# Kernel tuning notes

Measured on AMD Instinct MI355X. Metric: run time of the kernel, lower is better.

## Reference

```python
import jax, jax.numpy as jnp
import numpy as np

K = 20
EPS = 1e-5


def _bn(h, g, b, axes):
    m = jnp.mean(h, axes, keepdims=True)
    v = jnp.var(h, axes, keepdims=True)
    return (h - m) * jax.lax.rsqrt(v + EPS) * g + b


def _edge_feat(h):
    # h: [B,N,D] -> edge features [B,N,K,2D] = concat(central, neighbor-central)
    sq = jnp.sum(h * h, -1)
    # negative squared pairwise distance (larger = closer)
    adj = 2.0 * jnp.einsum('bnd,bmd->bnm', h, h) - sq[:, :, None] - sq[:, None, :]
    idx = jax.lax.top_k(adj, K)[1]  # [B,N,K] nearest (incl. self)
    nbr = jax.vmap(lambda hb, ib: hb[ib])(h, idx)  # [B,N,K,D]
    ctr = jnp.broadcast_to(h[:, :, None, :], nbr.shape)
    return jnp.concatenate([ctr, nbr - ctr], -1)


def _edge_layer(h, W, b, g, be):
    # 1x1 conv over edge features, relu THEN batchnorm (matches torch: bn(relu(conv))), max over K
    ef = _edge_feat(h)
    z = jax.nn.relu(jnp.einsum('bnkc,oc->bnko', ef, W) + b)
    z = _bn(z, g, be, (0, 1, 2))
    return jnp.max(z, axis=2)  # [B,N,O]


def _c1d(h, W, b):
    return jnp.einsum('bcl,oc->bol', h, W) + b[None, :, None]


def _bnc(h, g, b):
    m = jnp.mean(h, (0, 2), keepdims=True)
    v = jnp.var(h, (0, 2), keepdims=True)
    return (h - m) * jax.lax.rsqrt(v + EPS) * g[None, :, None] + b[None, :, None]


def _forward(x, rand_grid, W1, b1, g1, be1, W2, b2, g2, be2, W3, b3, g3, be3,
             W4, b4, g4, be4, W5, b5, g5, be5, lW, lb, lg, lbe,
             dW1, db1, dg1, dbe1, dW2, db2, dg2, dbe2, dW3, db3, dg3, dbe3, dW4, db4):
    pts = jnp.transpose(x, (0, 2, 1))  # [B,N,3]
    x1 = _edge_layer(pts, W1, b1, g1, be1)   # [B,N,64]
    x2 = _edge_layer(x1, W2, b2, g2, be2)    # [B,N,64]
    x3 = _edge_layer(x2, W3, b3, g3, be3)    # [B,N,64]
    x4 = _edge_layer(x3, W4, b4, g4, be4)    # [B,N,128]
    cat = jnp.concatenate([x1, x2, x3, x4], -1)  # [B,N,320]
    z = jax.nn.relu(jnp.einsum('bnc,oc->bno', cat, W5) + b5)
    z = _bn(z, g5, be5, (0, 1))
    glob = jnp.max(z, axis=1)  # [B,1024]
    lat = glob @ lW.T + lb
    lat = jax.nn.relu(_bn(lat, lg, lbe, (0,)))  # [B,1024]
    B, C = lat.shape
    P = rand_grid.shape[2]
    y = jnp.concatenate([rand_grid, jnp.broadcast_to(lat[:, :, None], (B, C, P))], axis=1)  # [B,1026,P]
    h = jax.nn.relu(_bnc(_c1d(y, dW1, db1), dg1, dbe1))
    h = jax.nn.relu(_bnc(_c1d(h, dW2, db2), dg2, dbe2))
    h = jax.nn.relu(_bnc(_c1d(h, dW3, db3), dg3, dbe3))
    return jnp.tanh(_c1d(h, dW4, db4))  # [B,3,P]


def setup_inputs() -> dict:
    key = jax.random.key(0)
    ks = iter(jax.random.split(key, 64))
    B, N, BOT = 8, 2048, 1024
    D = BOT + 2  # 1026
    f32 = jnp.float32

    def w(o, c):
        return jax.random.normal(next(ks), (o, c), dtype=f32) * 0.05

    def bnp(c):
        return jnp.ones((c,), f32), jnp.zeros((c,), f32)

    inp = {
        'x': jax.random.normal(next(ks), (B, 3, N), dtype=f32),
        'rand_grid': jax.random.uniform(next(ks), (B, 2, N), dtype=f32),
    }
    enc = [(64, 6), (64, 128), (64, 128), (128, 128), (1024, 320)]
    for i, (o, c) in enumerate(enc, 1):
        inp[f'W{i}'] = w(o, c)
        inp[f'b{i}'] = jnp.zeros((o,), f32)
        inp[f'g{i}'], inp[f'be{i}'] = bnp(o)
    inp['lW'] = w(BOT, 1024)
    inp['lb'] = jnp.zeros((BOT,), f32)
    inp['lg'], inp['lbe'] = bnp(BOT)
    dec = [(D, D), (D // 2, D), (D // 4, D // 2), (3, D // 4)]
    for i, (o, c) in enumerate(dec, 1):
        inp[f'dW{i}'] = w(o, c)
        inp[f'db{i}'] = jnp.zeros((o,), f32)
        if i < 4:
            inp[f'dg{i}'], inp[f'dbe{i}'] = bnp(o)
    return inp


def reference(x, rand_grid, W1, b1, g1, be1, W2, b2, g2, be2, W3, b3, g3, be3,
              W4, b4, g4, be4, W5, b5, g5, be5, lW, lb, lg, lbe,
              dW1, db1, dg1, dbe1, dW2, db2, dg2, dbe2, dW3, db3, dg3, dbe3, dW4, db4):
    return _forward(x, rand_grid, W1, b1, g1, be1, W2, b2, g2, be2, W3, b3, g3, be3,
                    W4, b4, g4, be4, W5, b5, g5, be5, lW, lb, lg, lbe,
                    dW1, db1, dg1, dbe1, dW2, db2, dg2, dbe2, dW3, db3, dg3, dbe3, dW4, db4)
```

## Files before the change

kernel.cpp:

```cpp
#include <hip/hip_runtime.h>
#include <math.h>

constexpr int NB = 8;
constexpr int NN = 2048;
constexpr int NK = 20;
constexpr int NP = 2048;


__global__ void transpose_x_kernel(const float* __restrict__ x, float* __restrict__ pts) {
  int gid = blockIdx.x * 256 + threadIdx.x;
  if (gid >= NB * NN * 3) return;
  int c = gid % 3;
  int n = (gid / 3) % NN;
  int b = gid / (3 * NN);
  pts[gid] = x[(b * 3 + c) * NN + n];
}

__global__ void transpose_mat_ld(const float* __restrict__ src, float* __restrict__ dst, int R,
                                 int C, int ldd) {
  __shared__ float tile[32][33];
  int c0 = blockIdx.x * 32, r0 = blockIdx.y * 32;
  int tx = threadIdx.x & 31, ty = threadIdx.x >> 5;
  for (int i = ty; i < 32; i += 8) {
    int r = r0 + i, c = c0 + tx;
    tile[i][tx] = (r < R && c < C) ? src[(size_t)r * C + c] : 0.f;
  }
  __syncthreads();
  for (int i = ty; i < 32; i += 8) {
    int c = c0 + i, r = r0 + tx;
    if (r < R && c < C) dst[(size_t)c * ldd + r] = tile[tx][i];
  }
}

template <int D>
__global__ void knn_dist_kernel(const float* __restrict__ h, int ld, int coff, int b0,
                                float* __restrict__ dmat) {
  __shared__ float sc[64][4];
  __shared__ float sr[64][4];
  int t = threadIdx.x;
  int c0 = blockIdx.x * 64;
  int r0 = blockIdx.y * 512;
  int bz = blockIdx.z;
  const float* rows = h + ((size_t)(b0 + bz) * NN) * ld + coff;
  if (t < 192) {
    int r = t / 3, c = t - r * 3;
    sc[r][c] = rows[(size_t)(c0 + r) * ld + c];
  }
  int tx = t & 15, ty = t >> 4;
  for (int rt = 0; rt < 8; rt++) {
    int rr0 = r0 + rt * 64;
    __syncthreads();
    if (t < 192) {
      int r = t / 3, c = t - r * 3;
      sr[r][c] = rows[(size_t)(rr0 + r) * ld + c];
    }
    __syncthreads();
    float acc[4][4] = {};
    float ca[4][3], rb[4][3];
#pragma unroll
    for (int i = 0; i < 4; i++)
#pragma unroll
      for (int d = 0; d < 3; d++) ca[i][d] = sc[ty + 16 * i][d];
#pragma unroll
    for (int j = 0; j < 4; j++)
#pragma unroll
      for (int d = 0; d < 3; d++) rb[j][d] = sr[tx + 16 * j][d];
#pragma unroll
    for (int i = 0; i < 4; i++)
#pragma unroll
      for (int j = 0; j < 4; j++)
#pragma unroll
        for (int d = 0; d < 3; d++) {
          float dd = ca[i][d] - rb[j][d];
          acc[i][j] = fmaf(dd, dd, acc[i][j]);
        }
#pragma unroll
    for (int i = 0; i < 4; i++)
#pragma unroll
      for (int j = 0; j < 4; j++)
        dmat[((size_t)bz * NN + c0 + ty + 16 * i) * NN + rr0 + tx + 16 * j] = -acc[i][j];
  }
}

__global__ __launch_bounds__(256, 2) void knn_dist128_kernel(const float* __restrict__ h, int ld,
                                                             int coff, int b0,
                                                             float* __restrict__ dmat) {
  __shared__ float sc[16][132];
  __shared__ float sr[16][128];
  int t = threadIdx.x;
  int c0 = blockIdx.x * 128, r0 = blockIdx.y * 128;
  int bz = blockIdx.z;
  const float* rows = h + ((size_t)(b0 + bz) * NN) * ld + coff;
  int arow = t >> 1, ac = (t & 1) * 8;
  int tx = t & 15, ty = t >> 4;
  float acc[8][8] = {};
  float rA[8], rB[8];

  auto gload = [&](int d0) {
    const float* pc = &rows[(size_t)(c0 + arow) * ld + d0 + ac];
    float4 a0 = *(const float4*)pc;
    float4 a1 = *(const float4*)(pc + 4);
    rA[0] = a0.x; rA[1] = a0.y; rA[2] = a0.z; rA[3] = a0.w;
    rA[4] = a1.x; rA[5] = a1.y; rA[6] = a1.z; rA[7] = a1.w;
    const float* pr = &rows[(size_t)(r0 + arow) * ld + d0 + ac];
    float4 b0 = *(const float4*)pr;
    float4 b1 = *(const float4*)(pr + 4);
    rB[0] = b0.x; rB[1] = b0.y; rB[2] = b0.z; rB[3] = b0.w;
    rB[4] = b1.x; rB[5] = b1.y; rB[6] = b1.z; rB[7] = b1.w;
  };
  auto ldswrite = [&]() {
#pragma unroll
    for (int j = 0; j < 8; j++) {
      sc[ac + j][arow] = rA[j];
      sr[ac + j][arow] = rB[j];
    }
  };

  gload(0);
  for (int ks = 0; ks < 4; ks++) {
    __syncthreads();
    ldswrite();
    __syncthreads();
    if (ks + 1 < 4) gload((ks + 1) * 16);
#pragma unroll
    for (int d = 0; d < 16; d++) {
      float4 a0 = *(const float4*)&sc[d][ty * 4];
      float4 a1 = *(const float4*)&sc[d][64 + ty * 4];
      float4 b0 = *(const float4*)&sr[d][tx * 4];
      float4 b1 = *(const float4*)&sr[d][64 + tx * 4];
      float av[8] = {a0.x, a0.y, a0.z, a0.w, a1.x, a1.y, a1.z, a1.w};
      float bv[8] = {b0.x, b0.y, b0.z, b0.w, b1.x, b1.y, b1.z, b1.w};
#pragma unroll
      for (int i = 0; i < 8; i++)
#pragma unroll
        for (int j = 0; j < 8; j++) {
          float dd = av[i] - bv[j];
          acc[i][j] = fmaf(dd, dd, acc[i][j]);
        }
    }
  }
#pragma unroll
  for (int i = 0; i < 8; i++) {
    int c = c0 + (i < 4 ? ty * 4 + i : 64 + ty * 4 + (i - 4));
    float* dst = &dmat[((size_t)bz * NN + c) * NN + r0];
    float4 q0, q1;
    q0.x = -acc[i][0]; q0.y = -acc[i][1]; q0.z = -acc[i][2]; q0.w = -acc[i][3];
    q1.x = -acc[i][4]; q1.y = -acc[i][5]; q1.z = -acc[i][6]; q1.w = -acc[i][7];
    *(float4*)&dst[tx * 4] = q0;
    *(float4*)&dst[64 + tx * 4] = q1;
  }
}

__global__ void knn_topk_kernel(const float* __restrict__ dmat, int b0, int* __restrict__ idx) {
  int t = threadIdx.x;
  int l = t & 63;
  int w = t >> 6;
  int gr = blockIdx.x * 4 + w;
  int bz = gr >> 11;
  int n = gr & 2047;
  const float* row = dmat + ((size_t)bz * NN + n) * NN;
  float v[32];
#pragma unroll
  for (int j = 0; j < 32; j++) v[j] = row[j * 64 + l];
  int mykm = 0;
  for (int k = 0; k < NK; k++) {
    float bv = v[0];
    int bj = 0;
#pragma unroll
    for (int j = 1; j < 32; j++) {
      if (v[j] > bv) { bv = v[j]; bj = j; }
    }
    int gm = bj * 64 + l;
#pragma unroll
    for (int off = 32; off; off >>= 1) {
      float ov = __shfl_xor(bv, off, 64);
      int om = __shfl_xor(gm, off, 64);
      if (ov > bv || (ov == bv && om < gm)) { bv = ov; gm = om; }
    }
    if (l == k) mykm = gm;
    int jb = gm >> 6, lb = gm & 63;
#pragma unroll
    for (int j = 0; j < 32; j++)
      if (j == jb && l == lb) v[j] = -3e38f;
  }
  if (l < NK) idx[((size_t)((b0 + bz) * NN + n)) * NK + l] = mykm;
}

__global__ void weff_kernel(const float* __restrict__ W, int O, int D, float* __restrict__ Weff) {
  int i = blockIdx.x * 256 + threadIdx.x;
  if (i >= 2 * O * D) return;
  int o = i / D, d = i - o * D;
  float v;
  if (o < O) v = W[(size_t)o * 2 * D + d] - W[(size_t)o * 2 * D + D + d];
  else v = W[(size_t)(o - O) * 2 * D + D + d];
  Weff[i] = v;
}

template <int M2, int D>
__global__ __launch_bounds__(256, 4) void pgemm_kernel(const float* __restrict__ h, int ld,
                                                       int coff, const float* __restrict__ Weff,
                                                       const float* __restrict__ bias,
                                                       float* __restrict__ P) {
  constexpr int O = M2 / 2;
  constexpr int GRP = 256 / M2;
  constexpr int NR = 8 / GRP;
  __shared__ float sh[8][D == 3 ? 4 : 68];
  int t = threadIdx.x;
  int n0 = blockIdx.x * 8;
  const float* base = h + coff;
  if constexpr (D == 64) {
    if (t < 128) {
      int r = t >> 4, q = (t & 15) * 4;
      *(float4*)&sh[r][q] = *(const float4*)&base[(size_t)(n0 + r) * ld + q];
    }
  } else {
    if (t < 24) {
      int r = t / 3, c = t - r * 3;
      sh[r][c] = base[(size_t)(n0 + r) * ld + c];
    }
  }
  __syncthreads();
  int o = t % M2;
  int gi = t / M2;
  float acc[NR];
  float bz = (o < O) ? bias[o] : 0.f;
#pragma unroll
  for (int j = 0; j < NR; j++) acc[j] = bz;
  const float* wr = Weff + (size_t)o * D;
  if constexpr (D == 64) {
#pragma unroll
    for (int d4 = 0; d4 < 16; d4++) {
      float4 w4 = *(const float4*)&wr[d4 * 4];
#pragma unroll
      for (int j = 0; j < NR; j++) {
        float4 e4 = *(const float4*)&sh[gi * NR + j][d4 * 4];
        acc[j] = fmaf(w4.x, e4.x, acc[j]);
        acc[j] = fmaf(w4.y, e4.y, acc[j]);
        acc[j] = fmaf(w4.z, e4.z, acc[j]);
        acc[j] = fmaf(w4.w, e4.w, acc[j]);
      }
    }
  } else {
    float w0 = wr[0], w1 = wr[1], w2 = wr[2];
#pragma unroll
    for (int j = 0; j < NR; j++) {
      int r = gi * NR + j;
      acc[j] = fmaf(w0, sh[r][0], fmaf(w1, sh[r][1], fmaf(w2, sh[r][2], acc[j])));
    }
  }
#pragma unroll
  for (int j = 0; j < NR; j++)
    P[(size_t)(n0 + gi * NR + j) * M2 + o] = acc[j];
}

template <int O>
__global__ __launch_bounds__(256, 8) void combine_kernel(const float* __restrict__ P,
                                                         const int* __restrict__ idx,
                                                         float* __restrict__ zmax,
                                                         float* __restrict__ zmin,
                                                         float* __restrict__ psum,
                                                         float* __restrict__ psq) {
  constexpr int CPB = 256 / O;
  constexpr int M2 = 2 * O;
  __shared__ int sidx[CPB * NK];
  int t = threadIdx.x;
  int bn0 = blockIdx.x * CPB;
  if (t < CPB * NK) sidx[t] = idx[(size_t)bn0 * NK + t];
  __syncthreads();
  int g = t / O, o = t % O;
  int bn = bn0 + g;
  int b = bn >> 11;
  float p1 = P[(size_t)bn * M2 + o];
  const float* P2 = P + (size_t)b * NN * M2 + O + o;
  float s = 0.f, sq = 0.f, mx = -3e38f, mn = 3e38f;
#pragma unroll
  for (int k = 0; k < NK; k++) {
    int nb = sidx[g * NK + k];
    float z = fmaxf(p1 + P2[(size_t)nb * M2], 0.f);
    s += z;
    sq = fmaf(z, z, sq);
    mx = fmaxf(mx, z);
    mn = fminf(mn, z);
  }
  zmax[(size_t)bn * O + o] = mx;
  zmin[(size_t)bn * O + o] = mn;
  psum[(size_t)o * (NB * NN) + bn] = s;
  psq[(size_t)o * (NB * NN) + bn] = sq;
}

__global__ void edge_reduce_kernel(const float* __restrict__ psum, const float* __restrict__ psq,
                                   const float* __restrict__ g, const float* __restrict__ be,
                                   float* __restrict__ scale, float* __restrict__ shift,
                                   double inv_n) {
  int o = blockIdx.x, t = threadIdx.x;
  double s = 0.0, q = 0.0;
  const float* ps = psum + (size_t)o * (NB * NN);
  const float* pq = psq + (size_t)o * (NB * NN);
  for (int i = t; i < NB * NN; i += 256) { s += (double)ps[i]; q += (double)pq[i]; }
  __shared__ double rs[256], rq[256];
  rs[t] = s; rq[t] = q;
  __syncthreads();
  for (int st = 128; st; st >>= 1) {
    if (t < st) { rs[t] += rs[t + st]; rq[t] += rq[t + st]; }
    __syncthreads();
  }
  if (t == 0) {
    double mean = rs[0] * inv_n;
    double var = rq[0] * inv_n - mean * mean;
    double r = 1.0 / sqrt(var + 1e-5);
    double sc = (double)g[o] * r;
    scale[o] = (float)sc;
    shift[o] = (float)((double)be[o] - mean * sc);
  }
}

__global__ void edge_affine_kernel(const float* __restrict__ zmax, const float* __restrict__ zmin,
                                   const float* __restrict__ scale, const float* __restrict__ shift,
                                   float* __restrict__ cat, int O, int coff_out) {
  int gid = blockIdx.x * 256 + threadIdx.x;
  int o = gid % O;
  int bn = gid / O;
  float sc = scale[o];
  float v = (sc >= 0.f) ? zmax[gid] : zmin[gid];
  cat[(size_t)bn * 320 + coff_out + o] = fmaf(sc, v, shift[o]);
}

__global__ __launch_bounds__(256, 2) void gemm5_64_kernel(const float* __restrict__ cat,
                                                          const float* __restrict__ W5t,
                                                          const float* __restrict__ b5,
                                                          float* __restrict__ z5) {
  __shared__ float sA[16][64];
  __shared__ float sB[16][128];
  int t = threadIdx.x;
  int r0 = blockIdx.x * 64, m0 = blockIdx.y * 128;
  int arow = t & 63, acq = (t >> 6) * 4;
  int blr = t >> 4, blc = (t & 15) * 8;
  int tx = t & 15, ty = t >> 4;
  float acc[4][8] = {};
  float rA[4], rB[8];

  auto gload = [&](int c0) {
    float4 a = *(const float4*)&cat[(size_t)(r0 + arow) * 320 + c0 + acq];
    rA[0] = a.x; rA[1] = a.y; rA[2] = a.z; rA[3] = a.w;
    const float* pb = &W5t[(size_t)(c0 + blr) * 1024 + m0 + blc];
    float4 b0 = *(const float4*)pb;
    float4 b1 = *(const float4*)(pb + 4);
    rB[0] = b0.x; rB[1] = b0.y; rB[2] = b0.z; rB[3] = b0.w;
    rB[4] = b1.x; rB[5] = b1.y; rB[6] = b1.z; rB[7] = b1.w;
  };
  auto ldswrite = [&]() {
#pragma unroll
    for (int j = 0; j < 4; j++) sA[acq + j][arow] = rA[j];
    float4 w0, w1;
    w0.x = rB[0]; w0.y = rB[1]; w0.z = rB[2]; w0.w = rB[3];
    w1.x = rB[4]; w1.y = rB[5]; w1.z = rB[6]; w1.w = rB[7];
    *(float4*)&sB[blr][blc] = w0;
    *(float4*)&sB[blr][blc + 4] = w1;
  };

  gload(0);
  for (int kt = 0; kt < 20; kt++) {
    __syncthreads();
    ldswrite();
    __syncthreads();
    if (kt + 1 < 20) gload((kt + 1) * 16);
#pragma unroll
    for (int c = 0; c < 16; c++) {
      float4 a0 = *(const float4*)&sA[c][ty * 4];
      float4 b0 = *(const float4*)&sB[c][tx * 4];
      float4 b1 = *(const float4*)&sB[c][64 + tx * 4];
      float av[4] = {a0.x, a0.y, a0.z, a0.w};
      float bv[8] = {b0.x, b0.y, b0.z, b0.w, b1.x, b1.y, b1.z, b1.w};
#pragma unroll
      for (int i = 0; i < 4; i++)
#pragma unroll
        for (int j = 0; j < 8; j++) acc[i][j] = fmaf(av[i], bv[j], acc[i][j]);
    }
  }
  float bj[8];
#pragma unroll
  for (int j = 0; j < 8; j++)
    bj[j] = b5[m0 + (j < 4 ? tx * 4 + j : 64 + tx * 4 + (j - 4))];
#pragma unroll
  for (int i = 0; i < 4; i++) {
    int r = r0 + ty * 4 + i;
    float* dst = &z5[(size_t)r * 1024 + m0];
    float4 q0, q1;
    q0.x = fmaxf(acc[i][0] + bj[0], 0.f);
    q0.y = fmaxf(acc[i][1] + bj[1], 0.f);
    q0.z = fmaxf(acc[i][2] + bj[2], 0.f);
    q0.w = fmaxf(acc[i][3] + bj[3], 0.f);
    q1.x = fmaxf(acc[i][4] + bj[4], 0.f);
    q1.y = fmaxf(acc[i][5] + bj[5], 0.f);
    q1.z = fmaxf(acc[i][6] + bj[6], 0.f);
    q1.w = fmaxf(acc[i][7] + bj[7], 0.f);
    *(float4*)&dst[tx * 4] = q0;
    *(float4*)&dst[64 + tx * 4] = q1;
  }
}

__global__ void stats5_kernel(const float* __restrict__ z5, double* __restrict__ psum5,
                              double* __restrict__ psq5, float* __restrict__ pmax5,
                              float* __restrict__ pmin5) {
  int j = blockIdx.x, t = threadIdx.x;
  int row0 = j * 64;
  double s0 = 0, s1 = 0, s2 = 0, s3 = 0, q0 = 0, q1 = 0, q2 = 0, q3 = 0;
  float4 mx = {-3e38f, -3e38f, -3e38f, -3e38f}, mn = {3e38f, 3e38f, 3e38f, 3e38f};
  for (int r = 0; r < 64; r++) {
    float4 v = *(const float4*)&z5[(size_t)(row0 + r) * 1024 + t * 4];
    s0 += v.x; s1 += v.y; s2 += v.z; s3 += v.w;
    q0 += (double)v.x * v.x; q1 += (double)v.y * v.y;
    q2 += (double)v.z * v.z; q3 += (double)v.w * v.w;
    mx.x = fmaxf(mx.x, v.x); mx.y = fmaxf(mx.y, v.y); mx.z = fmaxf(mx.z, v.z); mx.w = fmaxf(mx.w, v.w);
    mn.x = fminf(mn.x, v.x); mn.y = fminf(mn.y, v.y); mn.z = fminf(mn.z, v.z); mn.w = fminf(mn.w, v.w);
  }
  size_t base = (size_t)j * 1024 + t * 4;
  psum5[base + 0] = s0; psum5[base + 1] = s1; psum5[base + 2] = s2; psum5[base + 3] = s3;
  psq5[base + 0] = q0; psq5[base + 1] = q1; psq5[base + 2] = q2; psq5[base + 3] = q3;
  *(float4*)&pmax5[base] = mx;
  *(float4*)&pmin5[base] = mn;
}

__global__ void reduce5_glob_kernel(const double* __restrict__ psum5, const double* __restrict__ psq5,
                                    const float* __restrict__ pmax5, const float* __restrict__ pmin5,
                                    const float* __restrict__ g5, const float* __restrict__ be5,
                                    float* __restrict__ glob) {
  int o = blockIdx.x * 256 + threadIdx.x;
  double s = 0.0, q = 0.0;
  for (int j = 0; j < 256; j++) {
    s += psum5[(size_t)j * 1024 + o];
    q += psq5[(size_t)j * 1024 + o];
  }
  double mean = s * (1.0 / 16384.0);
  double var = q * (1.0 / 16384.0) - mean * mean;
  double r = 1.0 / sqrt(var + 1e-5);
  double scd = (double)g5[o] * r;
  float sc = (float)scd;
  float sh = (float)((double)be5[o] - mean * scd);
  for (int b = 0; b < 8; b++) {
    float m;
    if (sc >= 0.f) {
      m = -3e38f;
      for (int jj = 0; jj < 32; jj++) m = fmaxf(m, pmax5[(size_t)(b * 32 + jj) * 1024 + o]);
    } else {
      m = 3e38f;
      for (int jj = 0; jj < 32; jj++) m = fminf(m, pmin5[(size_t)(b * 32 + jj) * 1024 + o]);
    }
    glob[b * 1024 + o] = fmaf(sc, m, sh);
  }
}

__global__ void fc_kernel(const float* __restrict__ in, const float* __restrict__ Wt, int ld,
                          int coff, const float* __restrict__ bias, float* __restrict__ out,
                          int Ci, int Co) {
  __shared__ float sin_[1024];
  __shared__ float red[8][32];
  int b = blockIdx.x, t = threadIdx.x;
  for (int e = t; e < Ci; e += 256) sin_[e] = in[(size_t)b * Ci + e];
  __syncthreads();
  int o = blockIdx.y * 32 + (t & 31);
  int cg = t >> 5;
  int cn = Ci / 8;
  float p = 0.f;
  if (o < Co) {
    for (int c = cg * cn; c < (cg + 1) * cn; c++)
      p = fmaf(Wt[(size_t)(c + coff) * ld + o], sin_[c], p);
  }
  red[cg][t & 31] = p;
  __syncthreads();
  if (cg == 0 && o < Co) {
    float s = red[0][t] + red[1][t] + red[2][t] + red[3][t] + red[4][t] + red[5][t] + red[6][t] +
              red[7][t];
    out[(size_t)b * Co + o] = s + bias[o];
  }
}

__global__ void lat_bn_kernel(const float* __restrict__ latp, const float* __restrict__ lg,
                              const float* __restrict__ lbe, float* __restrict__ lat) {
  int o = blockIdx.x * 256 + threadIdx.x;
  float v[8];
  double s = 0.0, q = 0.0;
  for (int b = 0; b < 8; b++) {
    v[b] = latp[b * 1024 + o];
    s += (double)v[b];
    q += (double)v[b] * (double)v[b];
  }
  double mean = s * 0.125;
  double var = q * 0.125 - mean * mean;
  double r = 1.0 / sqrt(var + 1e-5);
  double gd = (double)lg[o], bd = (double)lbe[o];
  for (int b = 0; b < 8; b++) {
    float z = (float)(((double)v[b] - mean) * r * gd + bd);
    lat[b * 1024 + o] = fmaxf(z, 0.f);
  }
}

__global__ void dec1_z_kernel(const float* __restrict__ rg, const float* __restrict__ dW1t,
                              const float* __restrict__ u, float* __restrict__ z1) {
  int bo = blockIdx.x;
  int b = bo / 1026;
  int o = bo - b * 1026;
  int t = threadIdx.x;
  float w0 = dW1t[o], w1 = dW1t[1026 + o], ub = u[bo];
  const float4* r0 = (const float4*)(rg + (size_t)b * 2 * NP);
  const float4* r1 = (const float4*)(rg + (size_t)b * 2 * NP + NP);
  float4* zr = (float4*)(z1 + (size_t)bo * NP);
  for (int i = t; i < NP / 4; i += 256) {
    float4 a = r0[i], c = r1[i], rr;
    rr.x = fmaf(w0, a.x, fmaf(w1, c.x, ub));
    rr.y = fmaf(w0, a.y, fmaf(w1, c.y, ub));
    rr.z = fmaf(w0, a.z, fmaf(w1, c.z, ub));
    rr.w = fmaf(w0, a.w, fmaf(w1, c.w, ub));
    zr[i] = rr;
  }
}

__global__ void dstats_kernel(const float* __restrict__ z, int C, const float* __restrict__ g,
                              const float* __restrict__ be, float* __restrict__ scale,
                              float* __restrict__ shift) {
  int o = blockIdx.x, t = threadIdx.x;
  double s = 0.0, q = 0.0;
  for (int b = 0; b < 8; b++) {
    const float4* row = (const float4*)(z + ((size_t)b * C + o) * NP);
    for (int i = t; i < NP / 4; i += 256) {
      float4 v = row[i];
      s += (double)v.x + (double)v.y + (double)v.z + (double)v.w;
      q += (double)v.x * v.x + (double)v.y * v.y + (double)v.z * v.z + (double)v.w * v.w;
    }
  }
  __shared__ double rs[256], rq[256];
  rs[t] = s; rq[t] = q;
  __syncthreads();
  for (int st = 128; st; st >>= 1) {
    if (t < st) { rs[t] += rs[t + st]; rq[t] += rq[t + st]; }
    __syncthreads();
  }
  if (t == 0) {
    double inv = 1.0 / (8.0 * NP);
    double mean = rs[0] * inv;
    double var = rq[0] * inv - mean * mean;
    double r = 1.0 / sqrt(var + 1e-5);
    double sc = (double)g[o] * r;
    scale[o] = (float)sc;
    shift[o] = (float)((double)be[o] - mean * sc);
  }
}

__global__ __launch_bounds__(256, 2) void dec_gemm64_kernel(
    const float* __restrict__ zin, const float* __restrict__ Wt, int ldA,
    const float* __restrict__ bias, const float* __restrict__ scale,
    const float* __restrict__ shift, float* __restrict__ zout, int Ci, int Co) {
  __shared__ float sA[16][64];
  __shared__ float sB[16][128];
  int t = threadIdx.x;
  int m0 = blockIdx.x * 64, p0 = blockIdx.y * 128, b = blockIdx.z;
  int lr = t >> 4, lcA = (t & 15) * 4, lcB = (t & 15) * 8;
  int tx = t & 15, ty = t >> 4;
  int numK = (Ci + 15) >> 4;
  float acc[4][8] = {};
  float rA[4], rB[8];

  auto gload = [&](int kt) {
    int c = kt * 16 + lr;
#pragma unroll
    for (int j = 0; j < 4; j++) rA[j] = 0.f;
#pragma unroll
    for (int j = 0; j < 8; j++) rB[j] = 0.f;
    if (c < Ci) {
      int mb = m0 + lcA;
      if (mb + 4 <= Co) {
        float4 a0 = *(const float4*)&Wt[(size_t)c * ldA + mb];
        rA[0] = a0.x; rA[1] = a0.y; rA[2] = a0.z; rA[3] = a0.w;
      } else {
#pragma unroll
        for (int j = 0; j < 4; j++)
          if (mb + j < Co) rA[j] = Wt[(size_t)c * ldA + mb + j];
      }
      float sc = scale[c], sh = shift[c];
      const float* src = &zin[((size_t)b * Ci + c) * NP + p0 + lcB];
      float4 z0 = *(const float4*)src;
      float4 z1 = *(const float4*)(src + 4);
      rB[0] = fmaxf(fmaf(sc, z0.x, sh), 0.f);
      rB[1] = fmaxf(fmaf(sc, z0.y, sh), 0.f);
      rB[2] = fmaxf(fmaf(sc, z0.z, sh), 0.f);
      rB[3] = fmaxf(fmaf(sc, z0.w, sh), 0.f);
      rB[4] = fmaxf(fmaf(sc, z1.x, sh), 0.f);
      rB[5] = fmaxf(fmaf(sc, z1.y, sh), 0.f);
      rB[6] = fmaxf(fmaf(sc, z1.z, sh), 0.f);
      rB[7] = fmaxf(fmaf(sc, z1.w, sh), 0.f);
    }
  };
  auto ldswrite = [&]() {
    float4 v0;
    v0.x = rA[0]; v0.y = rA[1]; v0.z = rA[2]; v0.w = rA[3];
    *(float4*)&sA[lr][lcA] = v0;
    float4 w0, w1;
    w0.x = rB[0]; w0.y = rB[1]; w0.z = rB[2]; w0.w = rB[3];
    w1.x = rB[4]; w1.y = rB[5]; w1.z = rB[6]; w1.w = rB[7];
    *(float4*)&sB[lr][lcB] = w0;
    *(float4*)&sB[lr][lcB + 4] = w1;
  };

  gload(0);
  for (int kt = 0; kt < numK; kt++) {
    __syncthreads();
    ldswrite();
    __syncthreads();
    if (kt + 1 < numK) gload(kt + 1);
#pragma unroll
    for (int c = 0; c < 16; c++) {
      float4 a0 = *(const float4*)&sA[c][ty * 4];
      float4 b0 = *(const float4*)&sB[c][tx * 4];
      float4 b1 = *(const float4*)&sB[c][64 + tx * 4];
      float av[4] = {a0.x, a0.y, a0.z, a0.w};
      float bv[8] = {b0.x, b0.y, b0.z, b0.w, b1.x, b1.y, b1.z, b1.w};
#pragma unroll
      for (int i = 0; i < 4; i++)
#pragma unroll
        for (int j = 0; j < 8; j++) acc[i][j] = fmaf(av[i], bv[j], acc[i][j]);
    }
  }
#pragma unroll
  for (int i = 0; i < 4; i++) {
    int m = m0 + ty * 4 + i;
    if (m < Co) {
      float bv = bias[m];
      float* dst = &zout[((size_t)b * Co + m) * NP + p0];
      float4 q0, q1;
      q0.x = acc[i][0] + bv; q0.y = acc[i][1] + bv;
      q0.z = acc[i][2] + bv; q0.w = acc[i][3] + bv;
      q1.x = acc[i][4] + bv; q1.y = acc[i][5] + bv;
      q1.z = acc[i][6] + bv; q1.w = acc[i][7] + bv;
      *(float4*)&dst[tx * 4] = q0;
      *(float4*)&dst[64 + tx * 4] = q1;
    }
  }
}

__global__ void dec_final_kernel(const float* __restrict__ z3, const float* __restrict__ dW4,
                                 const float* __restrict__ db4, const float* __restrict__ scale,
                                 const float* __restrict__ shift, float* __restrict__ out) {
  __shared__ float w4[3 * 256];
  __shared__ float sc[256], sh[256];
  __shared__ float red[4][64][3];
  int b = blockIdx.x, pc = blockIdx.y, t = threadIdx.x;
  for (int e = t; e < 768; e += 256) w4[e] = dW4[e];
  sc[t] = scale[t];
  sh[t] = shift[t];
  __syncthreads();
  int tp = t & 63, tc = t >> 6;
  int p = pc * 64 + tp;
  float a0 = 0.f, a1 = 0.f, a2 = 0.f;
  for (int c = tc * 64; c < tc * 64 + 64; c++) {
    float hv = fmaxf(fmaf(sc[c], z3[((size_t)(b * 256 + c)) * NP + p], sh[c]), 0.f);
    a0 = fmaf(w4[c], hv, a0);
    a1 = fmaf(w4[256 + c], hv, a1);
    a2 = fmaf(w4[512 + c], hv, a2);
  }
  red[tc][tp][0] = a0;
  red[tc][tp][1] = a1;
  red[tc][tp][2] = a2;
  __syncthreads();
  if (tc == 0) {
    a0 = red[0][tp][0] + red[1][tp][0] + red[2][tp][0] + red[3][tp][0];
    a1 = red[0][tp][1] + red[1][tp][1] + red[2][tp][1] + red[3][tp][1];
    a2 = red[0][tp][2] + red[1][tp][2] + red[2][tp][2] + red[3][tp][2];
    out[((size_t)b * 3 + 0) * NP + p] = tanhf(a0 + db4[0]);
    out[((size_t)b * 3 + 1) * NP + p] = tanhf(a1 + db4[1]);
    out[((size_t)b * 3 + 2) * NP + p] = tanhf(a2 + db4[2]);
  }
}


extern "C" void kernel_launch(void* const* d_in, const int* in_sizes, int n_in, void* d_out,
                              int out_size, void* d_ws, size_t ws_size, hipStream_t stream) {
  const float* x = (const float*)d_in[0];
  const float* rg = (const float*)d_in[1];
  const float* W1 = (const float*)d_in[2];
  const float* b1 = (const float*)d_in[3];
  const float* g1 = (const float*)d_in[4];
  const float* be1 = (const float*)d_in[5];
  const float* W2 = (const float*)d_in[6];
  const float* b2 = (const float*)d_in[7];
  const float* g2 = (const float*)d_in[8];
  const float* be2 = (const float*)d_in[9];
  const float* W3 = (const float*)d_in[10];
  const float* b3 = (const float*)d_in[11];
  const float* g3 = (const float*)d_in[12];
  const float* be3 = (const float*)d_in[13];
  const float* W4 = (const float*)d_in[14];
  const float* b4 = (const float*)d_in[15];
  const float* g4 = (const float*)d_in[16];
  const float* be4 = (const float*)d_in[17];
  const float* W5 = (const float*)d_in[18];
  const float* b5 = (const float*)d_in[19];
  const float* g5 = (const float*)d_in[20];
  const float* be5 = (const float*)d_in[21];
  const float* lW = (const float*)d_in[22];
  const float* lb = (const float*)d_in[23];
  const float* lg = (const float*)d_in[24];
  const float* lbe = (const float*)d_in[25];
  const float* dW1 = (const float*)d_in[26];
  const float* db1 = (const float*)d_in[27];
  const float* dg1 = (const float*)d_in[28];
  const float* dbe1 = (const float*)d_in[29];
  const float* dW2 = (const float*)d_in[30];
  const float* db2 = (const float*)d_in[31];
  const float* dg2 = (const float*)d_in[32];
  const float* dbe2 = (const float*)d_in[33];
  const float* dW3 = (const float*)d_in[34];
  const float* db3 = (const float*)d_in[35];
  const float* dg3 = (const float*)d_in[36];
  const float* dbe3 = (const float*)d_in[37];
  const float* dW4 = (const float*)d_in[38];
  const float* db4 = (const float*)d_in[39];
  float* out = (float*)d_out;

  float* ws = (float*)d_ws;
  size_t off = 0;
  auto alloc = [&](size_t n) {
    size_t r = off;
    off += (n + 255) & ~(size_t)255;
    return r;
  };
  size_t f_pts = alloc((size_t)NB * NN * 3);
  size_t f_uA = alloc(13959168);
  size_t f_cat = f_uA;
  size_t f_idx = f_cat + 5242880;
  size_t f_zmax = f_idx + 327680;
  size_t f_zmin = f_zmax + 2097152;
  size_t f_psum = f_zmin + 2097152;
  size_t f_psq = f_psum + 2097152;
  size_t f_z2 = f_uA;
  size_t f_uB = alloc(16809984);
  size_t f_z5 = f_uB, f_z1 = f_uB;
  float* dmat = ws + f_uB;
  float* P = ws + f_uB;
  size_t f_uC = alloc(4194304);
  double* ps5_d = (double*)(ws + f_uC);
  double* pq5_d = ps5_d + 262144;
  size_t f_pM5 = f_uC + 2097152;
  size_t f_pm5 = f_pM5 + 262144;
  size_t f_z3 = f_uC;
  size_t f_weff = alloc(256 * 64);
  size_t f_W5t = alloc(320 * 1024);
  size_t f_lWt = alloc(1024 * 1024);
  size_t f_dW1t = alloc((size_t)1026 * 1026);
  size_t f_dW2t = alloc((size_t)1026 * 516);
  size_t f_dW3t = alloc(513 * 256);
  size_t f_scale = alloc(2048);
  size_t f_shift = alloc(2048);
  size_t f_glob = alloc(8 * 1024);
  size_t f_latp = alloc(8 * 1024);
  size_t f_lat = alloc(8 * 1024);
  size_t f_u = alloc(8 * 1026);
  (void)ws_size;
  (void)in_sizes;
  (void)n_in;
  (void)out_size;

  float* cat = ws + f_cat;
  int* idxp = (int*)(ws + f_idx);
  float* zmax = ws + f_zmax;
  float* zmin = ws + f_zmin;
  float* psumf = ws + f_psum;
  float* psqf = ws + f_psq;
  float* weff = ws + f_weff;
  float* scale = ws + f_scale;
  float* shift = ws + f_shift;
  const double invn_e = 1.0 / (double)(NB * NN * NK);

  transpose_x_kernel<<<192, 256, 0, stream>>>(x, ws + f_pts);
  transpose_mat_ld<<<dim3(10, 32), 256, 0, stream>>>(W5, ws + f_W5t, 1024, 320, 1024);
  transpose_mat_ld<<<dim3(32, 32), 256, 0, stream>>>(lW, ws + f_lWt, 1024, 1024, 1024);
  transpose_mat_ld<<<dim3(33, 33), 256, 0, stream>>>(dW1, ws + f_dW1t, 1026, 1026, 1026);
  transpose_mat_ld<<<dim3(33, 17), 256, 0, stream>>>(dW2, ws + f_dW2t, 513, 1026, 516);
  transpose_mat_ld<<<dim3(17, 8), 256, 0, stream>>>(dW3, ws + f_dW3t, 256, 513, 256);

  auto run_knn = [&](const float* h, int ld, int coff, bool d64) {
    for (int bb0 = 0; bb0 < NB; bb0 += 4) {
      if (d64)
        knn_dist128_kernel<<<dim3(16, 16, 4), 256, 0, stream>>>(h, ld, coff, bb0, dmat);
      else
        knn_dist_kernel<3><<<dim3(32, 4, 4), 256, 0, stream>>>(h, ld, coff, bb0, dmat);
      knn_topk_kernel<<<2048, 256, 0, stream>>>(dmat, bb0, idxp);
    }
  };

  run_knn(ws + f_pts, 3, 0, false);
  weff_kernel<<<2, 256, 0, stream>>>(W1, 64, 3, weff);
  pgemm_kernel<128, 3><<<2048, 256, 0, stream>>>(ws + f_pts, 3, 0, weff, b1, P);
  combine_kernel<64><<<4096, 256, 0, stream>>>(P, idxp, zmax, zmin, psumf, psqf);
  edge_reduce_kernel<<<64, 256, 0, stream>>>(psumf, psqf, g1, be1, scale, shift, invn_e);
  edge_affine_kernel<<<NB * NN * 64 / 256, 256, 0, stream>>>(zmax, zmin, scale, shift, cat, 64, 0);
  run_knn(cat, 320, 0, true);
  weff_kernel<<<32, 256, 0, stream>>>(W2, 64, 64, weff);
  pgemm_kernel<128, 64><<<2048, 256, 0, stream>>>(cat, 320, 0, weff, b2, P);
  combine_kernel<64><<<4096, 256, 0, stream>>>(P, idxp, zmax, zmin, psumf, psqf);
  edge_reduce_kernel<<<64, 256, 0, stream>>>(psumf, psqf, g2, be2, scale, shift, invn_e);
  edge_affine_kernel<<<NB * NN * 64 / 256, 256, 0, stream>>>(zmax, zmin, scale, shift, cat, 64, 64);
  run_knn(cat, 320, 64, true);
  weff_kernel<<<32, 256, 0, stream>>>(W3, 64, 64, weff);
  pgemm_kernel<128, 64><<<2048, 256, 0, stream>>>(cat, 320, 64, weff, b3, P);
  combine_kernel<64><<<4096, 256, 0, stream>>>(P, idxp, zmax, zmin, psumf, psqf);
  edge_reduce_kernel<<<64, 256, 0, stream>>>(psumf, psqf, g3, be3, scale, shift, invn_e);
  edge_affine_kernel<<<NB * NN * 64 / 256, 256, 0, stream>>>(zmax, zmin, scale, shift, cat, 64, 128);
  run_knn(cat, 320, 128, true);
  weff_kernel<<<64, 256, 0, stream>>>(W4, 128, 64, weff);
  pgemm_kernel<256, 64><<<2048, 256, 0, stream>>>(cat, 320, 128, weff, b4, P);
  combine_kernel<128><<<8192, 256, 0, stream>>>(P, idxp, zmax, zmin, psumf, psqf);
  edge_reduce_kernel<<<128, 256, 0, stream>>>(psumf, psqf, g4, be4, scale, shift, invn_e);
  edge_affine_kernel<<<NB * NN * 128 / 256, 256, 0, stream>>>(zmax, zmin, scale, shift, cat, 128, 192);

  gemm5_64_kernel<<<dim3(256, 8), 256, 0, stream>>>(cat, ws + f_W5t, b5, ws + f_z5);
  stats5_kernel<<<256, 256, 0, stream>>>(ws + f_z5, ps5_d, pq5_d, ws + f_pM5, ws + f_pm5);
  reduce5_glob_kernel<<<4, 256, 0, stream>>>(ps5_d, pq5_d, ws + f_pM5, ws + f_pm5, g5, be5,
                                             ws + f_glob);
  fc_kernel<<<dim3(8, 32), 256, 0, stream>>>(ws + f_glob, ws + f_lWt, 1024, 0, lb, ws + f_latp,
                                             1024, 1024);
  lat_bn_kernel<<<4, 256, 0, stream>>>(ws + f_latp, lg, lbe, ws + f_lat);
  fc_kernel<<<dim3(8, 33), 256, 0, stream>>>(ws + f_lat, ws + f_dW1t, 1026, 2, db1, ws + f_u, 1024,
                                             1026);
  dec1_z_kernel<<<8 * 1026, 256, 0, stream>>>(rg, ws + f_dW1t, ws + f_u, ws + f_z1);
  dstats_kernel<<<1026, 256, 0, stream>>>(ws + f_z1, 1026, dg1, dbe1, scale, shift);
  dec_gemm64_kernel<<<dim3(9, 16, 8), 256, 0, stream>>>(ws + f_z1, ws + f_dW2t, 516, db2, scale,
                                                        shift, ws + f_z2, 1026, 513);
  dstats_kernel<<<513, 256, 0, stream>>>(ws + f_z2, 513, dg2, dbe2, scale, shift);
  dec_gemm64_kernel<<<dim3(4, 16, 8), 256, 0, stream>>>(ws + f_z2, ws + f_dW3t, 256, db3, scale,
                                                        shift, ws + f_z3, 513, 256);
  dstats_kernel<<<256, 256, 0, stream>>>(ws + f_z3, 256, dg3, dbe3, scale, shift);
  dec_final_kernel<<<dim3(8, 32), 256, 0, stream>>>(ws + f_z3, dW4, db4, scale, shift, out);
}
```

Before: 1.858 ms.

## Fuse 3-D kNN distance and top-k; swizzle decoder GEMM block order

The first-layer kNN on 3-D points now runs as a single kernel. It loads a whole batch's points into shared memory, each wave computes its point's 2048 distances in registers, and it selects the top 20 with wave-shuffle argmax. This removes the dense distance-matrix write and read and two launches per batch half. The decoder GEMMs also switch to a 1-D grid with a remapped block order so that groups of 8 consecutive blocks share the same M tile, for better L2 reuse of the weights. Trade-off: only 4 waves per block, each reloading the full point set from global memory, and 20 serial selection passes over 32 registers per lane.

```diff
diff --git a/kernel.cpp b/kernel.cpp
--- a/kernel.cpp
+++ b/kernel.cpp
@@ -32,54 +32,56 @@
   }
 }
 
-template <int D>
-__global__ void knn_dist_kernel(const float* __restrict__ h, int ld, int coff, int b0,
-                                float* __restrict__ dmat) {
-  __shared__ float sc[64][4];
-  __shared__ float sr[64][4];
+__global__ void knn3_fused_kernel(const float* __restrict__ pts, int* __restrict__ idx) {
+  __shared__ float sm[3][NN];
   int t = threadIdx.x;
-  int c0 = blockIdx.x * 64;
-  int r0 = blockIdx.y * 512;
-  int bz = blockIdx.z;
-  const float* rows = h + ((size_t)(b0 + bz) * NN) * ld + coff;
-  if (t < 192) {
-    int r = t / 3, c = t - r * 3;
-    sc[r][c] = rows[(size_t)(c0 + r) * ld + c];
-  }
-  int tx = t & 15, ty = t >> 4;
-  for (int rt = 0; rt < 8; rt++) {
-    int rr0 = r0 + rt * 64;
-    __syncthreads();
-    if (t < 192) {
-      int r = t / 3, c = t - r * 3;
-      sr[r][c] = rows[(size_t)(rr0 + r) * ld + c];
-    }
-    __syncthreads();
-    float acc[4][4] = {};
-    float ca[4][3], rb[4][3];
-#pragma unroll
-    for (int i = 0; i < 4; i++)
-#pragma unroll
-      for (int d = 0; d < 3; d++) ca[i][d] = sc[ty + 16 * i][d];
-#pragma unroll
-    for (int j = 0; j < 4; j++)
-#pragma unroll
-      for (int d = 0; d < 3; d++) rb[j][d] = sr[tx + 16 * j][d];
-#pragma unroll
-    for (int i = 0; i < 4; i++)
-#pragma unroll
-      for (int j = 0; j < 4; j++)
-#pragma unroll
-        for (int d = 0; d < 3; d++) {
-          float dd = ca[i][d] - rb[j][d];
-          acc[i][j] = fmaf(dd, dd, acc[i][j]);
-        }
-#pragma unroll
-    for (int i = 0; i < 4; i++)
-#pragma unroll
-      for (int j = 0; j < 4; j++)
-        dmat[((size_t)bz * NN + c0 + ty + 16 * i) * NN + rr0 + tx + 16 * j] = -acc[i][j];
-  }
+  int l = t & 63, w = t >> 6;
+  int gb = blockIdx.x;
+  int b = gb >> 9;
+  int n0 = (gb & 511) * 4;
+  const float* base = pts + (size_t)b * NN * 3;
+  for (int e = t; e < NN * 3; e += 256) {
+    int col = e / 3, d = e - col * 3;
+    sm[d][col] = base[e];
+  }
+  __syncthreads();
+  int n = n0 + w;
+  float c0 = sm[0][n], c1 = sm[1][n], c2 = sm[2][n];
+  float v[32];
+#pragma unroll
+  for (int j = 0; j < 32; j++) {
+    int col = j * 64 + l;
+    float d0 = c0 - sm[0][col];
+    float d1 = c1 - sm[1][col];
+    float d2 = c2 - sm[2][col];
+    float acc = 0.f;
+    acc = fmaf(d0, d0, acc);
+    acc = fmaf(d1, d1, acc);
+    acc = fmaf(d2, d2, acc);
+    v[j] = -acc;
+  }
+  int mykm = 0;
+  for (int k = 0; k < NK; k++) {
+    float bv = v[0];
+    int bj = 0;
+#pragma unroll
+    for (int j = 1; j < 32; j++) {
+      if (v[j] > bv) { bv = v[j]; bj = j; }
+    }
+    int gm = bj * 64 + l;
+#pragma unroll
+    for (int off = 32; off; off >>= 1) {
+      float ov = __shfl_xor(bv, off, 64);
+      int om = __shfl_xor(gm, off, 64);
+      if (ov > bv || (ov == bv && om < gm)) { bv = ov; gm = om; }
+    }
+    if (l == k) mykm = gm;
+    int jb = gm >> 6, lb = gm & 63;
+#pragma unroll
+    for (int j = 0; j < 32; j++)
+      if (j == jb && l == lb) v[j] = -3e38f;
+  }
+  if (l < NK) idx[((size_t)(b * NN + n)) * NK + l] = mykm;
 }
 
 __global__ __launch_bounds__(256, 2) void knn_dist128_kernel(const float* __restrict__ h, int ld,
@@ -546,14 +548,23 @@
   }
 }
 
-__global__ __launch_bounds__(256, 2) void dec_gemm64_kernel(
+template <int NMT>
+__global__ __launch_bounds__(256, 2) void dec_gemm64s_kernel(
     const float* __restrict__ zin, const float* __restrict__ Wt, int ldA,
     const float* __restrict__ bias, const float* __restrict__ scale,
     const float* __restrict__ shift, float* __restrict__ zout, int Ci, int Co) {
   __shared__ float sA[16][64];
   __shared__ float sB[16][128];
+  int bid = blockIdx.x;
+  int gl = bid & 7;
+  int q = bid >> 3;
+  int gh = q / NMT;
+  int mt = q - gh * NMT;
+  int g = gl + (gh << 3);
+  int pt = g & 15;
+  int b = g >> 4;
+  int m0 = mt * 64, p0 = pt * 128;
   int t = threadIdx.x;
-  int m0 = blockIdx.x * 64, p0 = blockIdx.y * 128, b = blockIdx.z;
   int lr = t >> 4, lcA = (t & 15) * 4, lcB = (t & 15) * 8;
   int tx = t & 15, ty = t >> 4;
   int numK = (Ci + 15) >> 4;
@@ -777,35 +788,32 @@
   transpose_mat_ld<<<dim3(33, 17), 256, 0, stream>>>(dW2, ws + f_dW2t, 513, 1026, 516);
   transpose_mat_ld<<<dim3(17, 8), 256, 0, stream>>>(dW3, ws + f_dW3t, 256, 513, 256);
 
-  auto run_knn = [&](const float* h, int ld, int coff, bool d64) {
+  auto run_knn64 = [&](const float* h, int coff) {
     for (int bb0 = 0; bb0 < NB; bb0 += 4) {
-      if (d64)
-        knn_dist128_kernel<<<dim3(16, 16, 4), 256, 0, stream>>>(h, ld, coff, bb0, dmat);
-      else
-        knn_dist_kernel<3><<<dim3(32, 4, 4), 256, 0, stream>>>(h, ld, coff, bb0, dmat);
+      knn_dist128_kernel<<<dim3(16, 16, 4), 256, 0, stream>>>(h, 320, coff, bb0, dmat);
       knn_topk_kernel<<<2048, 256, 0, stream>>>(dmat, bb0, idxp);
     }
   };
 
-  run_knn(ws + f_pts, 3, 0, false);
+  knn3_fused_kernel<<<NB * NN / 4, 256, 0, stream>>>(ws + f_pts, idxp);
   weff_kernel<<<2, 256, 0, stream>>>(W1, 64, 3, weff);
   pgemm_kernel<128, 3><<<2048, 256, 0, stream>>>(ws + f_pts, 3, 0, weff, b1, P);
   combine_kernel<64><<<4096, 256, 0, stream>>>(P, idxp, zmax, zmin, psumf, psqf);
   edge_reduce_kernel<<<64, 256, 0, stream>>>(psumf, psqf, g1, be1, scale, shift, invn_e);
   edge_affine_kernel<<<NB * NN * 64 / 256, 256, 0, stream>>>(zmax, zmin, scale, shift, cat, 64, 0);
-  run_knn(cat, 320, 0, true);
+  run_knn64(cat, 0);
   weff_kernel<<<32, 256, 0, stream>>>(W2, 64, 64, weff);
   pgemm_kernel<128, 64><<<2048, 256, 0, stream>>>(cat, 320, 0, weff, b2, P);
   combine_kernel<64><<<4096, 256, 0, stream>>>(P, idxp, zmax, zmin, psumf, psqf);
   edge_reduce_kernel<<<64, 256, 0, stream>>>(psumf, psqf, g2, be2, scale, shift, invn_e);
   edge_affine_kernel<<<NB * NN * 64 / 256, 256, 0, stream>>>(zmax, zmin, scale, shift, cat, 64, 64);
-  run_knn(cat, 320, 64, true);
+  run_knn64(cat, 64);
   weff_kernel<<<32, 256, 0, stream>>>(W3, 64, 64, weff);
   pgemm_kernel<128, 64><<<2048, 256, 0, stream>>>(cat, 320, 64, weff, b3, P);
   combine_kernel<64><<<4096, 256, 0, stream>>>(P, idxp, zmax, zmin, psumf, psqf);
   edge_reduce_kernel<<<64, 256, 0, stream>>>(psumf, psqf, g3, be3, scale, shift, invn_e);
   edge_affine_kernel<<<NB * NN * 64 / 256, 256, 0, stream>>>(zmax, zmin, scale, shift, cat, 64, 128);
-  run_knn(cat, 320, 128, true);
+  run_knn64(cat, 128);
   weff_kernel<<<64, 256, 0, stream>>>(W4, 128, 64, weff);
   pgemm_kernel<256, 64><<<2048, 256, 0, stream>>>(cat, 320, 128, weff, b4, P);
   combine_kernel<128><<<8192, 256, 0, stream>>>(P, idxp, zmax, zmin, psumf, psqf);
@@ -823,11 +831,11 @@
                                              1026);
   dec1_z_kernel<<<8 * 1026, 256, 0, stream>>>(rg, ws + f_dW1t, ws + f_u, ws + f_z1);
   dstats_kernel<<<1026, 256, 0, stream>>>(ws + f_z1, 1026, dg1, dbe1, scale, shift);
-  dec_gemm64_kernel<<<dim3(9, 16, 8), 256, 0, stream>>>(ws + f_z1, ws + f_dW2t, 516, db2, scale,
-                                                        shift, ws + f_z2, 1026, 513);
+  dec_gemm64s_kernel<9><<<9 * 128, 256, 0, stream>>>(ws + f_z1, ws + f_dW2t, 516, db2, scale,
+                                                     shift, ws + f_z2, 1026, 513);
   dstats_kernel<<<513, 256, 0, stream>>>(ws + f_z2, 513, dg2, dbe2, scale, shift);
-  dec_gemm64_kernel<<<dim3(4, 16, 8), 256, 0, stream>>>(ws + f_z2, ws + f_dW3t, 256, db3, scale,
-                                                        shift, ws + f_z3, 513, 256);
+  dec_gemm64s_kernel<4><<<4 * 128, 256, 0, stream>>>(ws + f_z2, ws + f_dW3t, 256, db3, scale,
+                                                     shift, ws + f_z3, 513, 256);
   dstats_kernel<<<256, 256, 0, stream>>>(ws + f_z3, 256, dg3, dbe3, scale, shift);
   dec_final_kernel<<<dim3(8, 32), 256, 0, stream>>>(ws + f_z3, dW4, db4, scale, shift, out);
 }
```

Result: no change. 1.827 ms (-1.7%).
